# Kernel tuning notes

Measured on AMD Instinct MI355X. Metric: run time of the kernel, lower is better.

Reference implementation:

```python
import jax, jax.numpy as jnp
import numpy as np

HEAD_SIZE = 64
INPUT_SIZE = 1024
B, T = 8, 2048


def setup_inputs() -> dict:
    key = jax.random.key(0)
    kx, kq, kk, kv = jax.random.split(key, 4)
    x = jax.random.normal(kx, (B, T, INPUT_SIZE), dtype=jnp.float32)
    s = 1.0 / np.sqrt(INPUT_SIZE)
    Wq = jax.random.uniform(kq, (INPUT_SIZE, HEAD_SIZE), minval=-s, maxval=s, dtype=jnp.float32)
    Wk = jax.random.uniform(kk, (INPUT_SIZE, HEAD_SIZE), minval=-s, maxval=s, dtype=jnp.float32)
    Wv = jax.random.uniform(kv, (INPUT_SIZE, HEAD_SIZE), minval=-s, maxval=s, dtype=jnp.float32)
    return {"x": x, "Wq": Wq, "Wk": Wk, "Wv": Wv}


def reference(x, Wq, Wk, Wv):
    # Faithful to the torch module: scores = K @ Q^T (note: keys times queries^T),
    # causal mask on upper triangle of that matrix, softmax over last axis,
    # dropout treated as identity (eval), then scores @ V.
    q = jnp.einsum('bti,ih->bth', x, Wq)  # [B,T,H]
    k = jnp.einsum('bti,ih->bth', x, Wk)
    v = jnp.einsum('bti,ih->bth', x, Wv)
    scale = HEAD_SIZE ** -0.5
    scores = jnp.einsum('bth,bsh->bts', k, q) * scale  # [B,T,T] = K Q^T
    Tlen = x.shape[1]
    causal = jnp.tril(jnp.ones((Tlen, Tlen), dtype=bool))
    scores = jnp.where(causal, scores, -jnp.inf)
    w = jax.nn.softmax(scores, axis=-1)
    out = jnp.einsum('bts,bsh->bth', w, v)  # [B,T,H]
    return out
```

## Files before the change

### kernel.cpp

```cpp
#include <hip/hip_runtime.h>

typedef __bf16 bf16_t;
typedef bf16_t bf16x8 __attribute__((ext_vector_type(8)));
typedef float f32x4 __attribute__((ext_vector_type(4)));

#define NB 8
#define TT 2048
#define DIN 1024
#define HH 64
#define MM (NB * TT)

__device__ __forceinline__ unsigned short f2bf(float f) {
    unsigned int u = __float_as_uint(f);
    u += 0x7fffu + ((u >> 16) & 1u);
    return (unsigned short)(u >> 16);
}

__device__ __forceinline__ void async16(void* l, const void* g) {
    __builtin_amdgcn_global_load_lds(
        (const __attribute__((address_space(1))) unsigned int*)g,
        (__attribute__((address_space(3))) unsigned int*)l, 16, 0, 0);
}

__device__ __forceinline__ int block_detect_f32(const unsigned int* __restrict__ xw,
                                                int tid, int* sflag) {
    if (tid < 64) {
        unsigned int u = xw[tid];
        unsigned int e = (u >> 7) & 0xFFu;
        unsigned long long m = __ballot(e >= 100u && e <= 150u);
        if (tid == 0) *sflag = (__popcll(m) < 48) ? 1 : 0;
    }
    __syncthreads();
    return *sflag;
}

__global__ __launch_bounds__(256) void transpose_w_kernel(
    const void* __restrict__ Wq, const void* __restrict__ Wk,
    const void* __restrict__ Wv, const unsigned int* __restrict__ xw,
    unsigned short* __restrict__ Wt) {
    __shared__ int sflag;
    __shared__ unsigned short ts[64][68];
    const int tid = threadIdx.x;
    const int isf32 = block_detect_f32(xw, tid, &sflag);
    const int w = blockIdx.x >> 4, kt = blockIdx.x & 15;
    const void* W = (w == 0) ? Wq : (w == 1) ? Wk : Wv;
    const int kk = tid >> 4, nn = (tid & 15) * 4;
#pragma unroll
    for (int j = 0; j < 4; ++j) {
        int k = kk + j * 16;
        if (isf32) {
            float4 f = *(const float4*)((const float*)W + (size_t)(kt * 64 + k) * 64 + nn);
            ts[k][nn + 0] = f2bf(f.x); ts[k][nn + 1] = f2bf(f.y);
            ts[k][nn + 2] = f2bf(f.z); ts[k][nn + 3] = f2bf(f.w);
        } else {
            *(uint2*)&ts[k][nn] =
                *(const uint2*)((const unsigned short*)W + (size_t)(kt * 64 + k) * 64 + nn);
        }
    }
    __syncthreads();
    const int n = tid >> 2, k0 = (tid & 3) * 16;
    unsigned short tmp[16];
#pragma unroll
    for (int j = 0; j < 16; ++j) tmp[j] = ts[k0 + j][n];
    unsigned short* dst = Wt + (size_t)(w * 64 + n) * 1024 + kt * 64 + k0;
    *(uint4*)(dst + 0) = *(uint4*)&tmp[0];
    *(uint4*)(dst + 8) = *(uint4*)&tmp[8];
}

#define XR 72
#define WROWC 9

__global__ __launch_bounds__(256, 2) void proj_kernel(
    const void* __restrict__ xraw, const unsigned short* __restrict__ Wt,
    unsigned short* __restrict__ qbuf, unsigned short* __restrict__ kbuf,
    unsigned short* __restrict__ vtbuf) {
    __shared__ int sflag;
    __shared__ __align__(16) unsigned short xs[2][64 * XR];
    __shared__ __align__(16) unsigned char wlds[2][96 * WROWC * 16];

    const int tid = threadIdx.x;
    const int isf32 = block_detect_f32((const unsigned int*)xraw, tid, &sflag);
    const int bid = blockIdx.x;
    const int swz = (bid & 7) * 64 + (bid >> 3);
    const int nh = swz & 1;
    const int m0 = (swz >> 1) * 64;
    const int wave = tid >> 6, lane = tid & 63, quad = lane >> 4, l15 = lane & 15;
    const int rw = wave & 1, cw = wave >> 1;

    const float* xf = (const float*)xraw;
    const unsigned short* xb = (const unsigned short*)xraw;
    const unsigned char* wg = (const unsigned char*)Wt;

    const unsigned char* wsrc[4];
    unsigned int wdst[4];
    int nw = 0;
#pragma unroll
    for (int j = 0; j < 4; ++j) {
        int c = (wave + 4 * j) * 64 + lane;
        if (c < 864) {
            int R = c / WROWC, cc = c % WROWC;
            int ccu = (cc > 7) ? 0 : cc;
            wsrc[nw] = wg + (size_t)(nh * 96 + R) * 2048 + ccu * 16;
            wdst[nw] = c * 16;
            ++nw;
        }
    }

    const int xr = tid >> 2, xc = (tid & 3) * 16;
    float4 px[4];
    uint4  pxb[2];
    auto ldx = [&](int k0) {
        if (isf32) {
            const float* g = xf + (size_t)(m0 + xr) * DIN + k0 + xc;
#pragma unroll
            for (int j = 0; j < 4; ++j) px[j] = *(const float4*)(g + j * 4);
        } else {
            const unsigned short* g = xb + (size_t)(m0 + xr) * DIN + k0 + xc;
            pxb[0] = *(const uint4*)(g + 0);
            pxb[1] = *(const uint4*)(g + 8);
        }
    };
    auto writeX = [&](int buf) {
        if (isf32) {
            unsigned short t[16];
#pragma unroll
            for (int j = 0; j < 4; ++j) {
                t[j * 4 + 0] = f2bf(px[j].x); t[j * 4 + 1] = f2bf(px[j].y);
                t[j * 4 + 2] = f2bf(px[j].z); t[j * 4 + 3] = f2bf(px[j].w);
            }
            *(uint4*)&xs[buf][xr * XR + xc + 0] = *(uint4*)&t[0];
            *(uint4*)&xs[buf][xr * XR + xc + 8] = *(uint4*)&t[8];
        } else {
            *(uint4*)&xs[buf][xr * XR + xc + 0] = pxb[0];
            *(uint4*)&xs[buf][xr * XR + xc + 8] = pxb[1];
        }
    };
    auto stageW = [&](int buf, int itk) {
        const size_t off = (size_t)itk * 128;
        for (int j = 0; j < nw; ++j) async16(&wlds[buf][wdst[j]], wsrc[j] + off);
    };

    f32x4 acc[2][3];
#pragma unroll
    for (int rt = 0; rt < 2; ++rt)
#pragma unroll
        for (int ct = 0; ct < 3; ++ct)
            acc[rt][ct] = (f32x4){0.f, 0.f, 0.f, 0.f};

    auto compute = [&](int buf) {
#pragma unroll
        for (int ks = 0; ks < 2; ++ks) {
            bf16x8 a[2], b[3];
#pragma unroll
            for (int rt = 0; rt < 2; ++rt)
                a[rt] = *(const bf16x8*)
                    &xs[buf][(rw * 32 + rt * 16 + l15) * XR + ks * 32 + quad * 8];
#pragma unroll
            for (int ct = 0; ct < 3; ++ct)
                b[ct] = *(const bf16x8*)
                    &wlds[buf][(cw * 48 + ct * 16 + l15) * (WROWC * 16) + ks * 64 + quad * 16];
#pragma unroll
            for (int rt = 0; rt < 2; ++rt)
#pragma unroll
                for (int ct = 0; ct < 3; ++ct)
                    acc[rt][ct] = __builtin_amdgcn_mfma_f32_16x16x32_bf16(
                        a[rt], b[ct], acc[rt][ct], 0, 0, 0);
        }
    };

    ldx(0);
    writeX(0);
    stageW(0, 0);
    ldx(64);
    __syncthreads();

    for (int it = 0; it < 16; ++it) {
        if (it < 15) {
            writeX((it + 1) & 1);
            stageW((it + 1) & 1, it + 1);
            if (it < 14) ldx((it + 2) * 64);
        }
        compute(it & 1);
        __syncthreads();
    }

#pragma unroll
    for (int rt = 0; rt < 2; ++rt)
#pragma unroll
        for (int ct = 0; ct < 3; ++ct) {
            int n = nh * 96 + cw * 48 + ct * 16 + l15;
            int wsel = n >> 6, nn = n & 63;
#pragma unroll
            for (int reg = 0; reg < 4; ++reg) {
                int m = m0 + rw * 32 + rt * 16 + quad * 4 + reg;
                unsigned short bv = f2bf(acc[rt][ct][reg]);
                if (wsel == 0)      qbuf[(size_t)m * HH + nn] = bv;
                else if (wsel == 1) kbuf[(size_t)m * HH + nn] = bv;
                else {
                    int bb = m >> 11, t = m & 2047;
                    vtbuf[((size_t)bb * HH + nn) * TT + t] = bv;
                }
            }
        }
}

__global__ __launch_bounds__(256, 4) void attn_kernel(
    const unsigned short* __restrict__ rowbuf,
    const unsigned short* __restrict__ colbuf,
    const unsigned short* __restrict__ vtbuf,
    float* __restrict__ O_part,
    float* __restrict__ l_part) {

    __shared__ __align__(16) unsigned short Qr_s[64][72];
    __shared__ __align__(16) unsigned short Kc_s[64][72];
    __shared__ __align__(16) unsigned short Vt_s[64][72];
    __shared__ __align__(16) unsigned short P_s[4][16][72];

    const int tid  = threadIdx.x;
    const int bid  = blockIdx.x;
    const int b    = bid & 7;
    const int bx   = bid >> 3;
    int rt, ch;
    if (bx < 8)       { rt = bx;                 ch = 0; }
    else if (bx < 24) { rt = 8 + ((bx - 8) >> 1);  ch = (bx - 8) & 1; }
    else if (bx < 48) { rt = 16 + (bx - 24) / 3;   ch = (bx - 24) % 3; }
    else              { rt = 24 + ((bx - 48) >> 2); ch = (bx - 48) & 3; }
    const int nct = min(8, rt + 1 - ch * 8);
    const int t0 = rt * 64;
    const int slot = b * 80 + bx;

    const int wave = tid >> 6, lane = tid & 63, quad = lane >> 4, l15 = lane & 15;
    const int sr = tid >> 2, sc = (tid & 3) * 16;

    {
        const uint4* g = (const uint4*)(rowbuf + ((size_t)b * TT + t0 + sr) * HH + sc);
        *(uint4*)&Qr_s[sr][sc + 0] = g[0];
        *(uint4*)&Qr_s[sr][sc + 8] = g[1];
    }

    f32x4 o[4];
#pragma unroll
    for (int c = 0; c < 4; ++c) o[c] = (f32x4){0.f, 0.f, 0.f, 0.f};
    float ls[4] = {0.f, 0.f, 0.f, 0.f};

    const float SCL2 = 0.125f * 1.4426950408889634f;

    uint4 pk0, pk1, pv0, pv1;
    auto loadKV = [&](int i) {
        const int s0 = (ch * 8 + i) * 64;
        const uint4* gk = (const uint4*)(colbuf + ((size_t)b * TT + s0 + sr) * HH + sc);
        pk0 = gk[0]; pk1 = gk[1];
        const uint4* gv = (const uint4*)(vtbuf + ((size_t)b * HH + sr) * TT + s0 + sc);
        pv0 = gv[0]; pv1 = gv[1];
    };
    loadKV(0);

    for (int i = 0; i < nct; ++i) {
        const int stc = ch * 8 + i;
        const int s0 = stc * 64;
        *(uint4*)&Kc_s[sr][sc + 0] = pk0;
        *(uint4*)&Kc_s[sr][sc + 8] = pk1;
        *(uint4*)&Vt_s[sr][sc + 0] = pv0;
        *(uint4*)&Vt_s[sr][sc + 8] = pv1;
        __syncthreads();

        f32x4 scf[4];
#pragma unroll
        for (int c = 0; c < 4; ++c) scf[c] = (f32x4){0.f, 0.f, 0.f, 0.f};
#pragma unroll
        for (int ks = 0; ks < 2; ++ks) {
            bf16x8 a = *(const bf16x8*)&Qr_s[wave * 16 + l15][ks * 32 + quad * 8];
#pragma unroll
            for (int c = 0; c < 4; ++c) {
                bf16x8 bb = *(const bf16x8*)&Kc_s[c * 16 + l15][ks * 32 + quad * 8];
                scf[c] = __builtin_amdgcn_mfma_f32_16x16x32_bf16(a, bb, scf[c], 0, 0, 0);
            }
        }

        if (i + 1 < nct) loadKV(i + 1);

        const bool diag = (stc == rt);
#pragma unroll
        for (int r = 0; r < 4; ++r) {
            const int tg = t0 + wave * 16 + quad * 4 + r;
#pragma unroll
            for (int c = 0; c < 4; ++c) {
                float arg = fmaf(scf[c][r], SCL2, -30.f);
                if (diag && (s0 + c * 16 + l15) > tg) arg = -200.f;
                float p = __builtin_amdgcn_exp2f(arg);
                P_s[wave][quad * 4 + r][c * 16 + l15] = f2bf(p);
                ls[r] += p;
            }
        }
#pragma unroll
        for (int ks = 0; ks < 2; ++ks) {
            bf16x8 ap = *(const bf16x8*)&P_s[wave][l15][ks * 32 + quad * 8];
#pragma unroll
            for (int c = 0; c < 4; ++c) {
                bf16x8 bv = *(const bf16x8*)&Vt_s[c * 16 + l15][ks * 32 + quad * 8];
                o[c] = __builtin_amdgcn_mfma_f32_16x16x32_bf16(ap, bv, o[c], 0, 0, 0);
            }
        }
        __syncthreads();
    }

#pragma unroll
    for (int r = 0; r < 4; ++r) {
#pragma unroll
        for (int off = 1; off < 16; off <<= 1) ls[r] += __shfl_xor(ls[r], off);
    }
    if (l15 == 0) {
#pragma unroll
        for (int r = 0; r < 4; ++r)
            l_part[(size_t)slot * 64 + wave * 16 + quad * 4 + r] = ls[r];
    }
#pragma unroll
    for (int c = 0; c < 4; ++c)
#pragma unroll
        for (int r = 0; r < 4; ++r)
            O_part[(size_t)slot * 4096 + (wave * 16 + quad * 4 + r) * 64 + c * 16 + l15] = o[c][r];
}

__global__ __launch_bounds__(256) void combine_kernel(
    const float* __restrict__ O_part, const float* __restrict__ l_part,
    const unsigned int* __restrict__ xw, void* __restrict__ outraw) {
    __shared__ int sflag;
    const int tid = threadIdx.x;
    const int isf32 = block_detect_f32(xw, tid, &sflag);
    const int bid = blockIdx.x;
    const int b = bid & 7, rt = bid >> 3;
    const int nch = rt / 8 + 1;
    const int off = (rt < 8) ? rt : (rt < 16) ? 8 + 2 * (rt - 8)
                   : (rt < 24) ? 24 + 3 * (rt - 16) : 48 + 4 * (rt - 24);
    const int slot0 = b * 80 + off;

    const int row = tid >> 2, cb = (tid & 3) * 16;
    f32x4 a[4];
#pragma unroll
    for (int q = 0; q < 4; ++q) a[q] = (f32x4){0.f, 0.f, 0.f, 0.f};
    float l = 0.f;
    for (int j = 0; j < nch; ++j) {
        const f32x4* p = (const f32x4*)(O_part + (size_t)(slot0 + j) * 4096 + row * 64 + cb);
#pragma unroll
        for (int q = 0; q < 4; ++q) a[q] += p[q];
        l += l_part[(size_t)(slot0 + j) * 64 + row];
    }
    const float inv = 1.f / l;
    const size_t base = ((size_t)b * TT + rt * 64 + row) * HH + cb;
    if (isf32) {
        float* outf = (float*)outraw;
#pragma unroll
        for (int q = 0; q < 4; ++q) {
            f32x4 v = a[q] * inv;
            *(f32x4*)(outf + base + q * 4) = v;
        }
    } else {
        unsigned short h[16];
#pragma unroll
        for (int q = 0; q < 4; ++q)
#pragma unroll
            for (int e = 0; e < 4; ++e) h[q * 4 + e] = f2bf(a[q][e] * inv);
        unsigned short* outb = (unsigned short*)outraw;
        *(uint4*)(outb + base + 0) = *(uint4*)&h[0];
        *(uint4*)(outb + base + 8) = *(uint4*)&h[8];
    }
}

extern "C" void kernel_launch(void* const* d_in, const int* in_sizes, int n_in,
                              void* d_out, int out_size, void* d_ws, size_t ws_size,
                              hipStream_t stream) {
    const void* x  = d_in[0];
    const void* Wq = d_in[1];
    const void* Wk = d_in[2];
    const void* Wv = d_in[3];
    unsigned short* ws = (unsigned short*)d_ws;

    unsigned short* qbuf  = ws;
    unsigned short* kbuf  = ws + (size_t)MM * HH;
    unsigned short* vtbuf = ws + (size_t)2 * MM * HH;
    unsigned short* wtbuf = ws + (size_t)3 * MM * HH;
    float* O_part = (float*)(ws + (size_t)3 * MM * HH + 3 * 65536);
    float* l_part = O_part + (size_t)640 * 4096;

    hipLaunchKernelGGL(transpose_w_kernel, dim3(48), dim3(256), 0, stream,
                       Wq, Wk, Wv, (const unsigned int*)x, wtbuf);
    hipLaunchKernelGGL(proj_kernel, dim3(512), dim3(256), 0, stream,
                       x, wtbuf, qbuf, kbuf, vtbuf);
    hipLaunchKernelGGL(attn_kernel, dim3(640), dim3(256), 0, stream,
                       kbuf, qbuf, vtbuf, O_part, l_part);
    hipLaunchKernelGGL(combine_kernel, dim3(256), dim3(256), 0, stream,
                       O_part, l_part, (const unsigned int*)x, d_out);
}
```

Measured before the change: 175.4 us.

## Single-buffer projection LDS for higher occupancy and add MFMA priority hints in attention

The projection kernel drops its double-buffered LDS tiles for single buffers and raises launch bounds from 2 to 4 blocks per CU. Global x loads stay two iterations ahead in registers, but each step now needs two barriers. The block swizzle is replaced by a plain 2D grid. The attention kernel wraps its MFMA sections in s_setprio to favour matrix work over other waves, which may change how waves interleave.

```diff
diff --git a/kernel.cpp b/kernel.cpp
--- a/kernel.cpp
+++ b/kernel.cpp
@@ -70,20 +70,18 @@
 #define XR 72
 #define WROWC 9
 
-__global__ __launch_bounds__(256, 2) void proj_kernel(
+__global__ __launch_bounds__(256, 4) void proj_kernel(
     const void* __restrict__ xraw, const unsigned short* __restrict__ Wt,
     unsigned short* __restrict__ qbuf, unsigned short* __restrict__ kbuf,
     unsigned short* __restrict__ vtbuf) {
     __shared__ int sflag;
-    __shared__ __align__(16) unsigned short xs[2][64 * XR];
-    __shared__ __align__(16) unsigned char wlds[2][96 * WROWC * 16];
+    __shared__ __align__(16) unsigned short xs[64 * XR];
+    __shared__ __align__(16) unsigned char wlds[96 * WROWC * 16];
 
     const int tid = threadIdx.x;
     const int isf32 = block_detect_f32((const unsigned int*)xraw, tid, &sflag);
-    const int bid = blockIdx.x;
-    const int swz = (bid & 7) * 64 + (bid >> 3);
-    const int nh = swz & 1;
-    const int m0 = (swz >> 1) * 64;
+    const int m0 = blockIdx.x * 64;
+    const int nh = blockIdx.y;
     const int wave = tid >> 6, lane = tid & 63, quad = lane >> 4, l15 = lane & 15;
     const int rw = wave & 1, cw = wave >> 1;
 
@@ -107,9 +105,8 @@
     }
 
     const int xr = tid >> 2, xc = (tid & 3) * 16;
-    float4 px[4];
-    uint4  pxb[2];
-    auto ldx = [&](int k0) {
+
+    auto ldx = [&](int k0, float4 (&px)[4], uint4 (&pxb)[2]) {
         if (isf32) {
             const float* g = xf + (size_t)(m0 + xr) * DIN + k0 + xc;
 #pragma unroll
@@ -120,7 +117,7 @@
             pxb[1] = *(const uint4*)(g + 8);
         }
     };
-    auto writeX = [&](int buf) {
+    auto writeX = [&](float4 (&px)[4], uint4 (&pxb)[2]) {
         if (isf32) {
             unsigned short t[16];
 #pragma unroll
@@ -128,16 +125,12 @@
                 t[j * 4 + 0] = f2bf(px[j].x); t[j * 4 + 1] = f2bf(px[j].y);
                 t[j * 4 + 2] = f2bf(px[j].z); t[j * 4 + 3] = f2bf(px[j].w);
             }
-            *(uint4*)&xs[buf][xr * XR + xc + 0] = *(uint4*)&t[0];
-            *(uint4*)&xs[buf][xr * XR + xc + 8] = *(uint4*)&t[8];
+            *(uint4*)&xs[xr * XR + xc + 0] = *(uint4*)&t[0];
+            *(uint4*)&xs[xr * XR + xc + 8] = *(uint4*)&t[8];
         } else {
-            *(uint4*)&xs[buf][xr * XR + xc + 0] = pxb[0];
-            *(uint4*)&xs[buf][xr * XR + xc + 8] = pxb[1];
-        }
-    };
-    auto stageW = [&](int buf, int itk) {
-        const size_t off = (size_t)itk * 128;
-        for (int j = 0; j < nw; ++j) async16(&wlds[buf][wdst[j]], wsrc[j] + off);
+            *(uint4*)&xs[xr * XR + xc + 0] = pxb[0];
+            *(uint4*)&xs[xr * XR + xc + 8] = pxb[1];
+        }
     };
 
     f32x4 acc[2][3];
@@ -147,18 +140,18 @@
         for (int ct = 0; ct < 3; ++ct)
             acc[rt][ct] = (f32x4){0.f, 0.f, 0.f, 0.f};
 
-    auto compute = [&](int buf) {
+    auto compute = [&]() {
 #pragma unroll
         for (int ks = 0; ks < 2; ++ks) {
             bf16x8 a[2], b[3];
 #pragma unroll
             for (int rt = 0; rt < 2; ++rt)
                 a[rt] = *(const bf16x8*)
-                    &xs[buf][(rw * 32 + rt * 16 + l15) * XR + ks * 32 + quad * 8];
+                    &xs[(rw * 32 + rt * 16 + l15) * XR + ks * 32 + quad * 8];
 #pragma unroll
             for (int ct = 0; ct < 3; ++ct)
                 b[ct] = *(const bf16x8*)
-                    &wlds[buf][(cw * 48 + ct * 16 + l15) * (WROWC * 16) + ks * 64 + quad * 16];
+                    &wlds[(cw * 48 + ct * 16 + l15) * (WROWC * 16) + ks * 64 + quad * 16];
 #pragma unroll
             for (int rt = 0; rt < 2; ++rt)
 #pragma unroll
@@ -168,20 +161,24 @@
         }
     };
 
-    ldx(0);
-    writeX(0);
-    stageW(0, 0);
-    ldx(64);
-    __syncthreads();
-
-    for (int it = 0; it < 16; ++it) {
-        if (it < 15) {
-            writeX((it + 1) & 1);
-            stageW((it + 1) & 1, it + 1);
-            if (it < 14) ldx((it + 2) * 64);
-        }
-        compute(it & 1);
+    auto step = [&](int it, float4 (&px)[4], uint4 (&pxb)[2]) {
         __syncthreads();
+        writeX(px, pxb);
+        const size_t off = (size_t)it * 128;
+        for (int j = 0; j < nw; ++j) async16(&wlds[wdst[j]], wsrc[j] + off);
+        __syncthreads();
+        if (it < 14) ldx((it + 2) * 64, px, pxb);
+        compute();
+    };
+
+    float4 pxA[4], pxB[4];
+    uint4  pbA[2], pbB[2];
+    ldx(0, pxA, pbA);
+    ldx(64, pxB, pbB);
+
+    for (int itp = 0; itp < 16; itp += 2) {
+        step(itp + 0, pxA, pbA);
+        step(itp + 1, pxB, pbB);
     }
 
 #pragma unroll
@@ -267,6 +264,7 @@
         f32x4 scf[4];
 #pragma unroll
         for (int c = 0; c < 4; ++c) scf[c] = (f32x4){0.f, 0.f, 0.f, 0.f};
+        __builtin_amdgcn_s_setprio(1);
 #pragma unroll
         for (int ks = 0; ks < 2; ++ks) {
             bf16x8 a = *(const bf16x8*)&Qr_s[wave * 16 + l15][ks * 32 + quad * 8];
@@ -276,6 +274,7 @@
                 scf[c] = __builtin_amdgcn_mfma_f32_16x16x32_bf16(a, bb, scf[c], 0, 0, 0);
             }
         }
+        __builtin_amdgcn_s_setprio(0);
 
         if (i + 1 < nct) loadKV(i + 1);
 
@@ -292,6 +291,7 @@
                 ls[r] += p;
             }
         }
+        __builtin_amdgcn_s_setprio(1);
 #pragma unroll
         for (int ks = 0; ks < 2; ++ks) {
             bf16x8 ap = *(const bf16x8*)&P_s[wave][l15][ks * 32 + quad * 8];
@@ -301,6 +301,7 @@
                 o[c] = __builtin_amdgcn_mfma_f32_16x16x32_bf16(ap, bv, o[c], 0, 0, 0);
             }
         }
+        __builtin_amdgcn_s_setprio(0);
         __syncthreads();
     }
 
@@ -384,7 +385,7 @@
 
     hipLaunchKernelGGL(transpose_w_kernel, dim3(48), dim3(256), 0, stream,
                        Wq, Wk, Wv, (const unsigned int*)x, wtbuf);
-    hipLaunchKernelGGL(proj_kernel, dim3(512), dim3(256), 0, stream,
+    hipLaunchKernelGGL(proj_kernel, dim3(256, 2), dim3(256), 0, stream,
                        x, wtbuf, qbuf, kbuf, vtbuf);
     hipLaunchKernelGGL(attn_kernel, dim3(640), dim3(256), 0, stream,
                        kbuf, qbuf, vtbuf, O_part, l_part);
```

After: 154.5 us. 1.14x faster.
